# Performance work log

Hardware: AMD Instinct MI355X
Metric: run time of the kernel (lower is better)

Reference implementation:

```python
import jax, jax.numpy as jnp
import numpy as np

ALPHA = 0.1  # cfg.model.mmd.attention_temperature
EPS = 1e-12


def _l2norm(x, axis=-1):
    return x / jnp.sqrt(jnp.sum(x * x, axis=axis, keepdims=True) + EPS)


def setup_inputs() -> dict:
    key = jax.random.key(0)
    k1, k2, k3, k4 = jax.random.split(key, 4)
    b, ng, nl, nf, c = 8, 5, 75, 196, 640
    return {
        "global_f": jax.random.normal(k1, (b, ng, c), dtype=jnp.float32),
        "local_f": jax.random.normal(k2, (b, nl, nf, c), dtype=jnp.float32),
        "Wq": jax.random.normal(k3, (c, c), dtype=jnp.float32) / np.sqrt(c),
        "Wk": jax.random.normal(k4, (c, c), dtype=jnp.float32) / np.sqrt(c),
    }


def reference(global_f, local_f, Wq, Wk):
    # AttentiveMMDPrompt.compute_attn_weight with dim=1, num_groups=1.
    b, ng, c = global_f.shape
    _, nl, nf, _ = local_f.shape
    # q/k projections (nn.Linear, no bias): x @ W^T
    g = jnp.einsum('bgc,dc->bgd', global_f, Wq)          # [b, ng, c]
    l = jnp.einsum('blfc,dc->blfd', local_f, Wk)         # [b, nl, nf, c]
    # centering: subtract joint per-episode mean feature over all tokens
    tot = g.sum(axis=1) + l.sum(axis=(1, 2))             # [b, c]
    mean = tot / (ng + nl * nf)
    g = g - mean[:, None, :]
    l = l - mean[:, None, None, :]
    # l2 normalize feature vectors
    g = _l2norm(g)
    l = _l2norm(l)
    # score: local_f @ global_f -> [b, nl, ng, nf]
    scores = jnp.einsum('blfc,bgc->blgf', l, g) / ALPHA
    attn = jax.nn.softmax(scores, axis=-1)               # softmax over nf
    return attn[..., None]                               # [b, nl, ng, nf, 1]
```

## Files before the change

kernel.cpp:

```cpp
#include <hip/hip_runtime.h>
#include <math.h>

namespace {
constexpr int kB = 8, kNG = 5, kNL = 75, kNF = 196, kC = 640;
constexpr int kNTokL = kNL * kNF;
constexpr int kNTot = kNG + kNTokL;
constexpr float kEps = 1e-12f;
constexpr float kInvAlpha = 10.0f;
constexpr int kKC = 20;
constexpr int kTiles = 230;
}

typedef __attribute__((ext_vector_type(8))) short short8;
typedef __attribute__((ext_vector_type(4))) float floatx4;

union S8U { short8 v; ushort u[8]; };

__device__ __forceinline__ void bsplit(float x, ushort& h, ushort& l) {
  union { float f; uint u; } a; a.f = x;
  uint uh = (a.u + 0x7FFFu + ((a.u >> 16) & 1u)) >> 16;
  h = (ushort)uh;
  union { uint u; float f; } bb; bb.u = uh << 16;
  float r = x - bb.f;
  union { float f; uint u; } c; c.f = r;
  l = (ushort)((c.u + 0x7FFFu + ((c.u >> 16) & 1u)) >> 16);
}

#define MFMA_BF16(a, b, c) __builtin_amdgcn_mfma_f32_16x16x32_bf16(a, b, c, 0, 0, 0)

__device__ __forceinline__ void bar_lds() {
  asm volatile("s_waitcnt lgkmcnt(0)\n\ts_barrier" ::: "memory");
}


__global__ void k_sum_local(const float* __restrict__ lf, float* __restrict__ s_l) {
  const int b = blockIdx.x, s = blockIdx.y, c = threadIdx.x;
  const int t0 = s * 460, t1 = min(t0 + 460, kNTokL);
  const float* p = lf + ((size_t)b * kNTokL) * kC + c;
  float acc = 0.f;
  for (int t = t0; t < t1; ++t) acc += p[(size_t)t * kC];
  atomicAdd(&s_l[b * kC + c], acc);
}

__global__ void k_cvtW(const float* __restrict__ Wk, ushort* __restrict__ Wh,
                       ushort* __restrict__ Wl) {
  const int wv = blockIdx.x * 4 + (threadIdx.x >> 6);
  const int lane = threadIdx.x & 63;
  const int kc = wv % kKC, dt = wv / kKC;
  const int fm = lane & 15, quad = lane >> 4;
  const float* p = Wk + (size_t)(dt * 16 + fm) * kC + kc * 32 + quad * 8;
  float4 a = *(const float4*)p;
  float4 c = *(const float4*)(p + 4);
  S8U h, l;
  bsplit(a.x, h.u[0], l.u[0]); bsplit(a.y, h.u[1], l.u[1]);
  bsplit(a.z, h.u[2], l.u[2]); bsplit(a.w, h.u[3], l.u[3]);
  bsplit(c.x, h.u[4], l.u[4]); bsplit(c.y, h.u[5], l.u[5]);
  bsplit(c.z, h.u[6], l.u[6]); bsplit(c.w, h.u[7], l.u[7]);
  const size_t off = ((size_t)dt * kKC + kc) * 512 + (size_t)lane * 8;
  *(short8*)(Wh + off) = h.v;
  *(short8*)(Wl + off) = l.v;
}

__global__ void k_proj_mean(const float* __restrict__ Wq, const float* __restrict__ Wk,
                            const float* __restrict__ gf, const float* __restrict__ s_l,
                            float* __restrict__ m, float* __restrict__ gc) {
  const int wid = blockIdx.x * 4 + (threadIdx.x >> 6);
  const int lane = threadIdx.x & 63;
  const int b = wid / kC, d = wid % kC;
  float ak = 0.f, ag[kNG] = {0.f, 0.f, 0.f, 0.f, 0.f};
  for (int c = lane; c < kC; c += 64) {
    const float wq = Wq[d * kC + c];
    const float wk = Wk[d * kC + c];
    ak += wk * s_l[b * kC + c];
#pragma unroll
    for (int g = 0; g < kNG; ++g) ag[g] += wq * gf[(b * kNG + g) * kC + c];
  }
#pragma unroll
  for (int off = 32; off > 0; off >>= 1) {
    ak += __shfl_xor(ak, off);
#pragma unroll
    for (int g = 0; g < kNG; ++g) ag[g] += __shfl_xor(ag[g], off);
  }
  if (lane == 0) {
    float aq = 0.f;
#pragma unroll
    for (int g = 0; g < kNG; ++g) aq += ag[g];
    const float mv = (aq + ak) / (float)kNTot;
    m[b * kC + d] = mv;
#pragma unroll
    for (int g = 0; g < kNG; ++g) gc[(b * kNG + g) * kC + d] = ag[g] - mv;
  }
}

__global__ void k_norm_g(const float* __restrict__ gc, float* __restrict__ gn) {
  const int row = blockIdx.x;
  __shared__ float red[256];
  float a = 0.f;
  for (int d = threadIdx.x; d < kC; d += 256) {
    const float v = gc[row * kC + d];
    a += v * v;
  }
  red[threadIdx.x] = a;
  __syncthreads();
  for (int s = 128; s > 0; s >>= 1) {
    if (threadIdx.x < s) red[threadIdx.x] += red[threadIdx.x + s];
    __syncthreads();
  }
  const float rs = 1.0f / sqrtf(red[0] + kEps);
  for (int d = threadIdx.x; d < kC; d += 256) gn[row * kC + d] = gc[row * kC + d] * rs;
}

__global__ __launch_bounds__(256, 2) void k_big(
    const float* __restrict__ lf, const ushort* __restrict__ Wh,
    const ushort* __restrict__ Wl, const float* __restrict__ m,
    const float* __restrict__ gn, float* __restrict__ scores) {
  __shared__ char smem[8192];
  ushort* Ah = (ushort*)smem;
  ushort* Al = (ushort*)(smem + 4096);
  float* red = (float*)smem;

  const int tid = threadIdx.x;
  const int wn = tid >> 6, lane = tid & 63;
  const int fm = lane & 15, quad = lane >> 4;
  const int b = blockIdx.x & 7, tile = blockIdx.x >> 3;
  const int tok0 = tile * 64;

  const int sr = tid >> 2, sq = tid & 3;
  const int st = tok0 + sr;
  const bool sok = st < kNTokL;
  const float* xrow = lf + ((size_t)b * kNTokL + st) * kC + sq * 8;
  ushort* ah_w = Ah + (sr >> 4) * 512 + (size_t)(sq * 16 + (sr & 15)) * 8;
  ushort* al_w = Al + (sr >> 4) * 512 + (size_t)(sq * 16 + (sr & 15)) * 8;

  const ushort* bhbase = Wh + ((size_t)wn * 10 * kKC) * 512 + (size_t)lane * 8;
  const ushort* blbase = Wl + ((size_t)wn * 10 * kKC) * 512 + (size_t)lane * 8;

  floatx4 acc[4][10];
#pragma unroll
  for (int i = 0; i < 4; ++i)
#pragma unroll
    for (int j = 0; j < 10; ++j) acc[i][j] = (floatx4){0.f, 0.f, 0.f, 0.f};

  float4 xa = {0.f, 0.f, 0.f, 0.f}, xb = {0.f, 0.f, 0.f, 0.f};
  if (sok) { xa = *(const float4*)xrow; xb = *(const float4*)(xrow + 4); }

  for (int kc = 0; kc < kKC; ++kc) {
    const float4 ca = xa, cb = xb;
    if (kc + 1 < kKC && sok) {
      xa = *(const float4*)(xrow + (kc + 1) * 32);
      xb = *(const float4*)(xrow + (kc + 1) * 32 + 4);
    }
    short8 bh_n = *(const short8*)(bhbase + (size_t)kc * 512);
    short8 bl_n = *(const short8*)(blbase + (size_t)kc * 512);

    bar_lds();
    {
      S8U h, l;
      bsplit(ca.x, h.u[0], l.u[0]); bsplit(ca.y, h.u[1], l.u[1]);
      bsplit(ca.z, h.u[2], l.u[2]); bsplit(ca.w, h.u[3], l.u[3]);
      bsplit(cb.x, h.u[4], l.u[4]); bsplit(cb.y, h.u[5], l.u[5]);
      bsplit(cb.z, h.u[6], l.u[6]); bsplit(cb.w, h.u[7], l.u[7]);
      *(short8*)ah_w = h.v;
      *(short8*)al_w = l.v;
    }
    bar_lds();

    short8 ah[4], al[4];
#pragma unroll
    for (int mt = 0; mt < 4; ++mt) {
      ah[mt] = *(const short8*)(Ah + mt * 512 + (size_t)lane * 8);
      al[mt] = *(const short8*)(Al + mt * 512 + (size_t)lane * 8);
    }
#pragma unroll
    for (int nt = 0; nt < 10; ++nt) {
      const short8 bh_c = bh_n, bl_c = bl_n;
      if (nt + 1 < 10) {
        bh_n = *(const short8*)(bhbase + (size_t)((nt + 1) * kKC + kc) * 512);
        bl_n = *(const short8*)(blbase + (size_t)((nt + 1) * kKC + kc) * 512);
      }
#pragma unroll
      for (int mt = 0; mt < 4; ++mt) {
        acc[mt][nt] = MFMA_BF16(ah[mt], bh_c, acc[mt][nt]);
        acc[mt][nt] = MFMA_BF16(al[mt], bh_c, acc[mt][nt]);
        acc[mt][nt] = MFMA_BF16(ah[mt], bl_c, acc[mt][nt]);
      }
    }
  }

  float mv[10], gvv[5][10];
#pragma unroll
  for (int nt = 0; nt < 10; ++nt) {
    const int d = wn * 160 + nt * 16 + fm;
    mv[nt] = m[b * kC + d];
#pragma unroll
    for (int g = 0; g < 5; ++g) gvv[g][nt] = gn[(b * kNG + g) * kC + d];
  }

  bar_lds();
#pragma unroll
  for (int mt = 0; mt < 4; ++mt)
#pragma unroll
    for (int reg = 0; reg < 4; ++reg) {
      float part[6] = {0.f, 0.f, 0.f, 0.f, 0.f, 0.f};
#pragma unroll
      for (int nt = 0; nt < 10; ++nt) {
        const float yc = acc[mt][nt][reg] - mv[nt];
        part[0] += yc * yc;
#pragma unroll
        for (int g = 0; g < 5; ++g) part[1 + g] += yc * gvv[g][nt];
      }
#pragma unroll
      for (int off = 1; off < 16; off <<= 1)
#pragma unroll
        for (int v = 0; v < 6; ++v) part[v] += __shfl_xor(part[v], off);
      if (fm == 0) {
        const int row = mt * 16 + quad * 4 + reg;
#pragma unroll
        for (int v = 0; v < 6; ++v) red[((size_t)wn * 64 + row) * 6 + v] = part[v];
      }
    }
  bar_lds();
  if (tid < 64) {
    const int tok = tok0 + tid;
    if (tok < kNTokL) {
      float s[6] = {0.f, 0.f, 0.f, 0.f, 0.f, 0.f};
#pragma unroll
      for (int w = 0; w < 4; ++w)
#pragma unroll
        for (int v = 0; v < 6; ++v) s[v] += red[((size_t)w * 64 + tid) * 6 + v];
      const float rs = (1.0f / sqrtf(s[0] + kEps)) * kInvAlpha;
      const size_t t = (size_t)b * kNTokL + tok;
#pragma unroll
      for (int g = 0; g < 5; ++g)
        scores[(size_t)g * (kB * kNTokL) + t] = s[1 + g] * rs;
    }
  }
}

__global__ void k_softmax(const float* __restrict__ scores, float* __restrict__ out) {
  const int wid = blockIdx.x * 4 + (threadIdx.x >> 6);
  const int lane = threadIdx.x & 63;
  const int b = wid / (kNL * kNG);
  const int rem = wid % (kNL * kNG);
  const int l = rem / kNG, g = rem % kNG;
  float sv[4];
  float mx = -1e30f;
#pragma unroll
  for (int u = 0; u < 4; ++u) {
    const int f = lane + 64 * u;
    if (f < kNF) {
      const size_t t = (size_t)b * kNTokL + (size_t)l * kNF + f;
      sv[u] = scores[(size_t)g * (kB * kNTokL) + t];
      mx = fmaxf(mx, sv[u]);
    } else {
      sv[u] = 0.f;
    }
  }
#pragma unroll
  for (int off = 32; off > 0; off >>= 1) mx = fmaxf(mx, __shfl_xor(mx, off));
  float se = 0.f;
#pragma unroll
  for (int u = 0; u < 4; ++u) {
    const int f = lane + 64 * u;
    const float e = (f < kNF) ? expf(sv[u] - mx) : 0.f;
    sv[u] = e;
    se += e;
  }
#pragma unroll
  for (int off = 32; off > 0; off >>= 1) se += __shfl_xor(se, off);
  const float inv = 1.0f / se;
#pragma unroll
  for (int u = 0; u < 4; ++u) {
    const int f = lane + 64 * u;
    if (f < kNF) out[((size_t)(b * kNL + l) * kNG + g) * kNF + f] = sv[u] * inv;
  }
}


extern "C" void kernel_launch(void* const* d_in, const int* in_sizes, int n_in,
                              void* d_out, int out_size, void* d_ws, size_t ws_size,
                              hipStream_t stream) {
  (void)in_sizes; (void)n_in; (void)out_size; (void)ws_size;
  const float* gf = (const float*)d_in[0];
  const float* lf = (const float*)d_in[1];
  const float* Wq = (const float*)d_in[2];
  const float* Wk = (const float*)d_in[3];
  float* ws = (float*)d_ws;
  float* out = (float*)d_out;

  float* s_l    = ws;
  float* m      = ws + 5120;
  float* gc     = ws + 10240;
  float* gn     = ws + 35840;
  float* scores = ws + 61440;
  ushort* Wh    = (ushort*)(ws + 649440);
  ushort* Wl    = (ushort*)(ws + 854240);

  hipMemsetAsync(s_l, 0, (size_t)5120 * 4, stream);

  k_sum_local<<<dim3(kB, 32), kC, 0, stream>>>(lf, s_l);
  k_cvtW<<<200, 256, 0, stream>>>(Wk, Wh, Wl);
  k_proj_mean<<<(kB * kC) / 4, 256, 0, stream>>>(Wq, Wk, gf, s_l, m, gc);
  k_norm_g<<<kB * kNG, 256, 0, stream>>>(gc, gn);
  k_big<<<kTiles * kB, 256, 0, stream>>>(lf, Wh, Wl, m, gn, scores);
  k_softmax<<<750, 256, 0, stream>>>(scores, out);
}
```

Before: 891.5 us.

## Double-buffer A tiles in k_big with 8 waves and vectorize local-sum reduction

The main GEMM kernel now runs 512 threads (8 waves, each covering 5 N-tiles instead of 10) and double-buffers the bf16 hi/lo A tiles in LDS. This cuts the barrier count per K step and overlaps staging of the next chunk with the MFMA work. B fragments for a whole K chunk are prefetched into registers. The local-sum kernel now uses float4 loads over more slices. The trade-off is lower occupancy with launch bounds of (512,1), which raises register pressure.

```diff
diff --git a/kernel.cpp b/kernel.cpp
--- a/kernel.cpp
+++ b/kernel.cpp
@@ -9,12 +9,15 @@
 constexpr float kInvAlpha = 10.0f;
 constexpr int kKC = 20;
 constexpr int kTiles = 230;
+constexpr int kNT = 5;
 }
 
 typedef __attribute__((ext_vector_type(8))) short short8;
+typedef __attribute__((ext_vector_type(4))) short short4v;
 typedef __attribute__((ext_vector_type(4))) float floatx4;
 
 union S8U { short8 v; ushort u[8]; };
+union S4U { short4v v; ushort u[4]; };
 
 __device__ __forceinline__ void bsplit(float x, ushort& h, ushort& l) {
   union { float f; uint u; } a; a.f = x;
@@ -34,12 +37,22 @@
 
 
 __global__ void k_sum_local(const float* __restrict__ lf, float* __restrict__ s_l) {
-  const int b = blockIdx.x, s = blockIdx.y, c = threadIdx.x;
-  const int t0 = s * 460, t1 = min(t0 + 460, kNTokL);
-  const float* p = lf + ((size_t)b * kNTokL) * kC + c;
-  float acc = 0.f;
-  for (int t = t0; t < t1; ++t) acc += p[(size_t)t * kC];
-  atomicAdd(&s_l[b * kC + c], acc);
+  const int b = blockIdx.x, slice = blockIdx.y;
+  const int tid = threadIdx.x;
+  const int c4 = tid % 160, h = tid / 160;
+  const int t0 = slice * 230 + h * 115;
+  const int nrow = min(115, kNTokL - t0);
+  const float* p = lf + ((size_t)b * kNTokL + t0) * kC + c4 * 4;
+  float4 acc = {0.f, 0.f, 0.f, 0.f};
+  for (int i = 0; i < nrow; ++i) {
+    const float4 v = *(const float4*)(p + (size_t)i * kC);
+    acc.x += v.x; acc.y += v.y; acc.z += v.z; acc.w += v.w;
+  }
+  float* dst = &s_l[b * kC + c4 * 4];
+  atomicAdd(dst + 0, acc.x);
+  atomicAdd(dst + 1, acc.y);
+  atomicAdd(dst + 2, acc.z);
+  atomicAdd(dst + 3, acc.w);
 }
 
 __global__ void k_cvtW(const float* __restrict__ Wk, ushort* __restrict__ Wh,
@@ -110,13 +123,15 @@
   for (int d = threadIdx.x; d < kC; d += 256) gn[row * kC + d] = gc[row * kC + d] * rs;
 }
 
-__global__ __launch_bounds__(256, 2) void k_big(
+__global__ __launch_bounds__(512, 1) void k_big(
     const float* __restrict__ lf, const ushort* __restrict__ Wh,
     const ushort* __restrict__ Wl, const float* __restrict__ m,
     const float* __restrict__ gn, float* __restrict__ scores) {
-  __shared__ char smem[8192];
-  ushort* Ah = (ushort*)smem;
-  ushort* Al = (ushort*)(smem + 4096);
+  __shared__ char smem[16384];
+  ushort* Ah0 = (ushort*)smem;
+  ushort* Al0 = (ushort*)(smem + 4096);
+  ushort* Ah1 = (ushort*)(smem + 8192);
+  ushort* Al1 = (ushort*)(smem + 12288);
   float* red = (float*)smem;
 
   const int tid = threadIdx.x;
@@ -125,72 +140,89 @@
   const int b = blockIdx.x & 7, tile = blockIdx.x >> 3;
   const int tok0 = tile * 64;
 
-  const int sr = tid >> 2, sq = tid & 3;
+  const int sr = tid >> 3, sq = tid & 7;
   const int st = tok0 + sr;
   const bool sok = st < kNTokL;
-  const float* xrow = lf + ((size_t)b * kNTokL + st) * kC + sq * 8;
-  ushort* ah_w = Ah + (sr >> 4) * 512 + (size_t)(sq * 16 + (sr & 15)) * 8;
-  ushort* al_w = Al + (sr >> 4) * 512 + (size_t)(sq * 16 + (sr & 15)) * 8;
-
-  const ushort* bhbase = Wh + ((size_t)wn * 10 * kKC) * 512 + (size_t)lane * 8;
-  const ushort* blbase = Wl + ((size_t)wn * 10 * kKC) * 512 + (size_t)lane * 8;
-
-  floatx4 acc[4][10];
+  const float* xrow = lf + ((size_t)b * kNTokL + st) * kC + sq * 4;
+  const int aoff = ((sr >> 4) << 9) + (((sq >> 1) * 16 + (sr & 15)) << 3) + ((sq & 1) << 2);
+
+  const ushort* bhbase = Wh + ((size_t)wn * kNT * kKC) * 512 + (size_t)lane * 8;
+  const ushort* blbase = Wl + ((size_t)wn * kNT * kKC) * 512 + (size_t)lane * 8;
+
+  floatx4 acc[4][kNT];
 #pragma unroll
   for (int i = 0; i < 4; ++i)
 #pragma unroll
-    for (int j = 0; j < 10; ++j) acc[i][j] = (floatx4){0.f, 0.f, 0.f, 0.f};
-
-  float4 xa = {0.f, 0.f, 0.f, 0.f}, xb = {0.f, 0.f, 0.f, 0.f};
-  if (sok) { xa = *(const float4*)xrow; xb = *(const float4*)(xrow + 4); }
-
-  for (int kc = 0; kc < kKC; ++kc) {
-    const float4 ca = xa, cb = xb;
-    if (kc + 1 < kKC && sok) {
-      xa = *(const float4*)(xrow + (kc + 1) * 32);
-      xb = *(const float4*)(xrow + (kc + 1) * 32 + 4);
+    for (int j = 0; j < kNT; ++j) acc[i][j] = (floatx4){0.f, 0.f, 0.f, 0.f};
+
+#define STAGE_A(XV, AH, AL)                                   \
+  {                                                           \
+    S4U _h, _l;                                               \
+    bsplit((XV).x, _h.u[0], _l.u[0]);                         \
+    bsplit((XV).y, _h.u[1], _l.u[1]);                         \
+    bsplit((XV).z, _h.u[2], _l.u[2]);                         \
+    bsplit((XV).w, _h.u[3], _l.u[3]);                         \
+    *(short4v*)((AH) + aoff) = _h.v;                          \
+    *(short4v*)((AL) + aoff) = _l.v;                          \
+  }
+
+#define LOADB(BH, BL, KCI)                                                        \
+  {                                                                               \
+    _Pragma("unroll") for (int nt = 0; nt < kNT; ++nt) {                          \
+      BH[nt] = *(const short8*)(bhbase + ((size_t)nt * kKC + (KCI)) * 512);       \
+      BL[nt] = *(const short8*)(blbase + ((size_t)nt * kKC + (KCI)) * 512);       \
+    }                                                                             \
+  }
+
+#define READA(AH, AL)                                                  \
+  {                                                                    \
+    _Pragma("unroll") for (int mt = 0; mt < 4; ++mt) {                 \
+      ah[mt] = *(const short8*)((AH) + mt * 512 + lane * 8);           \
+      al[mt] = *(const short8*)((AL) + mt * 512 + lane * 8);           \
+    }                                                                  \
+  }
+
+#define DOMFMA(BH, BL)                                                 \
+  {                                                                    \
+    _Pragma("unroll") for (int nt = 0; nt < kNT; ++nt)                 \
+        _Pragma("unroll") for (int mt = 0; mt < 4; ++mt) {             \
+      acc[mt][nt] = MFMA_BF16(ah[mt], BH[nt], acc[mt][nt]);            \
+      acc[mt][nt] = MFMA_BF16(al[mt], BH[nt], acc[mt][nt]);            \
+      acc[mt][nt] = MFMA_BF16(ah[mt], BL[nt], acc[mt][nt]);            \
+    }                                                                  \
+  }
+
+  const float4 fzero = {0.f, 0.f, 0.f, 0.f};
+  float4 x0 = sok ? *(const float4*)xrow : fzero;
+  STAGE_A(x0, Ah0, Al0);
+  float4 xA = sok ? *(const float4*)(xrow + 32) : fzero;
+  float4 xB = fzero;
+  short8 BH0[kNT], BL0[kNT], BH1[kNT], BL1[kNT];
+  LOADB(BH0, BL0, 0);
+
+  short8 ah[4], al[4];
+  for (int kc = 0; kc < kKC; kc += 2) {
+    bar_lds();
+    READA(Ah0, Al0);
+    LOADB(BH1, BL1, kc + 1);
+    if (sok && kc + 2 < kKC) xB = *(const float4*)(xrow + (kc + 2) * 32);
+    STAGE_A(xA, Ah1, Al1);
+    DOMFMA(BH0, BL0);
+
+    bar_lds();
+    READA(Ah1, Al1);
+    if (kc + 2 < kKC) {
+      LOADB(BH0, BL0, kc + 2);
+      if (sok && kc + 3 < kKC) xA = *(const float4*)(xrow + (kc + 3) * 32);
+      STAGE_A(xB, Ah0, Al0);
     }
-    short8 bh_n = *(const short8*)(bhbase + (size_t)kc * 512);
-    short8 bl_n = *(const short8*)(blbase + (size_t)kc * 512);
-
-    bar_lds();
-    {
-      S8U h, l;
-      bsplit(ca.x, h.u[0], l.u[0]); bsplit(ca.y, h.u[1], l.u[1]);
-      bsplit(ca.z, h.u[2], l.u[2]); bsplit(ca.w, h.u[3], l.u[3]);
-      bsplit(cb.x, h.u[4], l.u[4]); bsplit(cb.y, h.u[5], l.u[5]);
-      bsplit(cb.z, h.u[6], l.u[6]); bsplit(cb.w, h.u[7], l.u[7]);
-      *(short8*)ah_w = h.v;
-      *(short8*)al_w = l.v;
-    }
-    bar_lds();
-
-    short8 ah[4], al[4];
-#pragma unroll
-    for (int mt = 0; mt < 4; ++mt) {
-      ah[mt] = *(const short8*)(Ah + mt * 512 + (size_t)lane * 8);
-      al[mt] = *(const short8*)(Al + mt * 512 + (size_t)lane * 8);
-    }
-#pragma unroll
-    for (int nt = 0; nt < 10; ++nt) {
-      const short8 bh_c = bh_n, bl_c = bl_n;
-      if (nt + 1 < 10) {
-        bh_n = *(const short8*)(bhbase + (size_t)((nt + 1) * kKC + kc) * 512);
-        bl_n = *(const short8*)(blbase + (size_t)((nt + 1) * kKC + kc) * 512);
-      }
-#pragma unroll
-      for (int mt = 0; mt < 4; ++mt) {
-        acc[mt][nt] = MFMA_BF16(ah[mt], bh_c, acc[mt][nt]);
-        acc[mt][nt] = MFMA_BF16(al[mt], bh_c, acc[mt][nt]);
-        acc[mt][nt] = MFMA_BF16(ah[mt], bl_c, acc[mt][nt]);
-      }
-    }
-  }
-
-  float mv[10], gvv[5][10];
-#pragma unroll
-  for (int nt = 0; nt < 10; ++nt) {
-    const int d = wn * 160 + nt * 16 + fm;
+    DOMFMA(BH1, BL1);
+  }
+
+  float mv[kNT], gvv[5][kNT];
+#pragma unroll
+  for (int nt = 0; nt < kNT; ++nt) {
+    const int d = wn * 80 + nt * 16 + fm;
     mv[nt] = m[b * kC + d];
 #pragma unroll
     for (int g = 0; g < 5; ++g) gvv[g][nt] = gn[(b * kNG + g) * kC + d];
@@ -203,7 +235,7 @@
     for (int reg = 0; reg < 4; ++reg) {
       float part[6] = {0.f, 0.f, 0.f, 0.f, 0.f, 0.f};
 #pragma unroll
-      for (int nt = 0; nt < 10; ++nt) {
+      for (int nt = 0; nt < kNT; ++nt) {
         const float yc = acc[mt][nt][reg] - mv[nt];
         part[0] += yc * yc;
 #pragma unroll
@@ -225,7 +257,7 @@
     if (tok < kNTokL) {
       float s[6] = {0.f, 0.f, 0.f, 0.f, 0.f, 0.f};
 #pragma unroll
-      for (int w = 0; w < 4; ++w)
+      for (int w = 0; w < 8; ++w)
 #pragma unroll
         for (int v = 0; v < 6; ++v) s[v] += red[((size_t)w * 64 + tid) * 6 + v];
       const float rs = (1.0f / sqrtf(s[0] + kEps)) * kInvAlpha;
@@ -235,6 +267,10 @@
         scores[(size_t)g * (kB * kNTokL) + t] = s[1 + g] * rs;
     }
   }
+#undef STAGE_A
+#undef LOADB
+#undef READA
+#undef DOMFMA
 }
 
 __global__ void k_softmax(const float* __restrict__ scores, float* __restrict__ out) {
@@ -298,10 +334,10 @@
 
   hipMemsetAsync(s_l, 0, (size_t)5120 * 4, stream);
 
-  k_sum_local<<<dim3(kB, 32), kC, 0, stream>>>(lf, s_l);
+  k_sum_local<<<dim3(kB, 64), 320, 0, stream>>>(lf, s_l);
   k_cvtW<<<200, 256, 0, stream>>>(Wk, Wh, Wl);
   k_proj_mean<<<(kB * kC) / 4, 256, 0, stream>>>(Wq, Wk, gf, s_l, m, gc);
   k_norm_g<<<kB * kNG, 256, 0, stream>>>(gc, gn);
-  k_big<<<kTiles * kB, 256, 0, stream>>>(lf, Wh, Wl, m, gn, scores);
+  k_big<<<kTiles * kB, 512, 0, stream>>>(lf, Wh, Wl, m, gn, scores);
   k_softmax<<<750, 256, 0, stream>>>(scores, out);
 }
```

New measurement: 766.1 us. 1.16x faster.
